# Performance work log

Measured on AMD Instinct MI355X. Metric: run time of the kernel, lower is better.

## Reference

```python
import jax, jax.numpy as jnp
import numpy as np

N_QUBITS = 8
N_LAYERS = 2


def _apply_1q(state, U, wire, n):
    # state: (bs, 2**n); U: (2,2) fixed or (bs,2,2) batched; wire 0 = most significant
    bs = state.shape[0]
    left = 2 ** wire
    right = 2 ** (n - wire - 1)
    s = state.reshape(bs, left, 2, right)
    if U.ndim == 2:
        s = jnp.einsum('ij,bljr->blir', U, s)
    else:
        s = jnp.einsum('bij,bljr->blir', U, s)
    return s.reshape(bs, -1)


def _apply_ctrl(state, U, control, target, n):
    # apply 2x2 U on `target` where `control` qubit is |1>
    bs = state.shape[0]
    left = 2 ** control
    right = 2 ** (n - control - 1)
    s = state.reshape(bs, left, 2, right)
    s0 = s[:, :, 0, :].reshape(bs, -1)
    s1 = s[:, :, 1, :].reshape(bs, -1)
    t = target if target < control else target - 1  # target index among remaining n-1 wires
    s1 = _apply_1q(s1, U, t, n - 1)
    s = jnp.stack([s0.reshape(bs, left, right), s1.reshape(bs, left, right)], axis=2)
    return s.reshape(bs, -1)


def _rz_batched(theta):
    h = 0.5 * theta
    c, s = jnp.cos(h), jnp.sin(h)
    z = jnp.zeros_like(c)
    row0 = jnp.stack([c - 1j * s, z + 0j], axis=-1)
    row1 = jnp.stack([z + 0j, c + 1j * s], axis=-1)
    return jnp.stack([row0, row1], axis=-2).astype(jnp.complex64)  # (bs,2,2)


def _ry_batched(theta):
    h = 0.5 * theta
    c, s = jnp.cos(h), jnp.sin(h)
    row0 = jnp.stack([c, -s], axis=-1)
    row1 = jnp.stack([s, c], axis=-1)
    return jnp.stack([row0, row1], axis=-2).astype(jnp.complex64)


def _rx_fixed(theta):
    h = 0.5 * theta
    c, s = jnp.cos(h), jnp.sin(h)
    return jnp.stack([jnp.stack([c + 0j, -1j * s]), jnp.stack([-1j * s, c + 0j])]).astype(jnp.complex64)


def _ry_fixed(theta):
    h = 0.5 * theta
    c, s = jnp.cos(h), jnp.sin(h)
    return jnp.stack([jnp.stack([c + 0j, -s + 0j]), jnp.stack([s + 0j, c + 0j])]).astype(jnp.complex64)


def _circuit(X, weights):
    bs, L = X.shape
    n = N_QUBITS
    vpq = L // n + 1  # var_per_qubit
    state = jnp.zeros((bs, 2 ** n), jnp.complex64).at[:, 0].set(1.0)
    H = jnp.asarray(np.array([[1, 1], [1, -1]], np.complex64) / np.sqrt(2))
    # encoding: Hadamard then alternating RZ/RY per qubit
    for q in range(n):
        state = _apply_1q(state, H, q, n)
        for i in range(vpq):
            idx = q * vpq + i
            if idx >= L:
                break
            th = X[:, idx]
            U = _rz_batched(th) if i % 2 == 0 else _ry_batched(th)
            state = _apply_1q(state, U, q, n)
    # entangling ring: layer 0 -> CRX, layer 1 -> CRY ((l+1)%2==0 -> CRY)
    for l in range(N_LAYERS):
        for i in range(n):
            th = weights[l, i]
            U = _ry_fixed(th) if (l + 1) % 2 == 0 else _rx_fixed(th)
            state = _apply_ctrl(state, U, i, (i + 1) % n, n)
    # PauliZ expectation on each wire
    p = state.real ** 2 + state.imag ** 2  # (bs, 256)
    outs = []
    for q in range(n):
        pq = p.reshape(bs, 2 ** q, 2, -1).sum(axis=(1, 3))  # (bs, 2)
        outs.append(pq[:, 0] - pq[:, 1])
    return jnp.stack(outs, axis=1)  # (bs, 8)


def setup_inputs() -> dict:
    key = jax.random.key(0)
    k1, k2 = jax.random.split(key)
    X = jax.random.normal(k1, (16384, 64), dtype=jnp.float32)
    weights = jax.random.normal(k2, (N_LAYERS, N_LAYERS * N_QUBITS), dtype=jnp.float32)
    return {"X": X, "weights": weights}


def reference(X, weights):
    return _circuit(X, weights)
```

## Files before the change

### kernel.cpp

```cpp
#include <hip/hip_runtime.h>

#define DEV __device__ __forceinline__
typedef float f32x2 __attribute__((ext_vector_type(2)));
typedef float f32x4 __attribute__((ext_vector_type(4)));

DEV float rdlane(float v, int l) {
  return __int_as_float(__builtin_amdgcn_readlane(__float_as_int(v), l));
}
DEV f32x2 pkfma(f32x2 a, f32x2 b, f32x2 c) { return __builtin_elementwise_fma(a, b, c); }
DEV f32x2 splat(float x) { return (f32x2){x, x}; }
DEV f32x2 swap2(f32x2 v) { return __builtin_shufflevector(v, v, 1, 0); }
DEV f32x2 cmul(f32x2 P, f32x2 F) {
  f32x2 t = swap2(P);
  f32x2 m = {-t.x, t.y};
  return pkfma(splat(F.y), m, splat(F.x) * P);
}

template <int CTRL>
DEV float dppmov(float v) {
  return __int_as_float(__builtin_amdgcn_update_dpp(
      0, __float_as_int(v), CTRL, 0xf, 0xf, true));
}
template <int M>
DEV float xorl(float v) {
  if constexpr (M == 1)       return dppmov<0xB1>(v);
  else if constexpr (M == 2)  return dppmov<0x4E>(v);
  else if constexpr (M == 8)  return dppmov<0x128>(v);
  else if constexpr (M == 4)
    return __int_as_float(__builtin_amdgcn_ds_swizzle(__float_as_int(v), 0x101F));
  else
    return __int_as_float(__builtin_amdgcn_ds_swizzle(__float_as_int(v), 0x401F));
}

template <int M, bool CRX, int R0, int RS>
DEV void gate_lane(f32x2 amp[8], int lane, float c1, float s1) {
  const f32x2 C2 = splat(c1);
  if constexpr (CRX) {
    const f32x2 S2 = {s1, -s1};
#pragma unroll
    for (int r = R0; r < 8; r += RS) {
      f32x2 p;
      p.x = xorl<M>(amp[r].y);
      p.y = xorl<M>(amp[r].x);
      amp[r] = pkfma(S2, p, C2 * amp[r]);
    }
  } else {
    const float sp = (lane & M) ? s1 : -s1;
    const f32x2 SP = splat(sp);
#pragma unroll
    for (int r = R0; r < 8; r += RS) {
      f32x2 p;
      p.x = xorl<M>(amp[r].x);
      p.y = xorl<M>(amp[r].y);
      amp[r] = pkfma(SP, p, C2 * amp[r]);
    }
  }
}

template <bool CRX>
DEV void gate_pair(f32x2& aI, f32x2& aJ, float c1, float s1) {
  const f32x2 C2 = splat(c1);
  f32x2 nI, nJ;
  if constexpr (CRX) {
    const f32x2 S2 = {s1, -s1};
    nI = pkfma(S2, swap2(aJ), C2 * aI);
    nJ = pkfma(S2, swap2(aI), C2 * aJ);
  } else {
    nI = pkfma(splat(-s1), aJ, C2 * aI);
    nJ = pkfma(splat(s1), aI, C2 * aJ);
  }
  aI = nI; aJ = nJ;
}

__global__ __launch_bounds__(256, 8) void qsim_kernel(const float* __restrict__ X,
                                                      const float* __restrict__ W,
                                                      float* __restrict__ out, int bs) {
  const int lane = threadIdx.x & 63;
  const int wave = blockIdx.x * (blockDim.x >> 6) + (threadIdx.x >> 6);
  const int b0 = wave * 2;
  if (b0 >= bs) return;

  float w = W[(((lane & 15) >> 3) << 4) + (lane & 7)];
  float sw, cw;
  __sincosf(0.5f * w, &sw, &cw);

  const int ce = (lane >> 3) & 1;
  const int cq = lane & 7;
  int bb = b0 + ce; bb = bb >= bs ? bs - 1 : bb;
  const float* Xrow = X + (size_t)bb * 64;
  float ang[9];
#pragma unroll
  for (int i = 0; i < 9; ++i) {
    int idx = cq * 9 + i;
    idx = idx > 63 ? 63 : idx;
    ang[i] = Xrow[idx];
  }
  const float Hc = 0.70710678118654752440f;
  f32x2 A = {Hc, 0.f}, B = {Hc, 0.f};
#pragma unroll
  for (int i = 0; i < 9; ++i) {
    float s, c;
    __sincosf(0.5f * ang[i], &s, &c);
    if (i > 0) {
      bool dead = (cq == 7);
      c = dead ? 1.f : c;
      s = dead ? 0.f : s;
    }
    if ((i & 1) == 0) {
      f32x2 nA = pkfma((f32x2){s, -s}, swap2(A), splat(c) * A);
      f32x2 nB = pkfma((f32x2){-s, s}, swap2(B), splat(c) * B);
      A = nA; B = nB;
    } else {
      f32x2 nA = pkfma(splat(-s), B, splat(c) * A);
      f32x2 nB = pkfma(splat(c), B, splat(s) * A);
      A = nA; B = nB;
    }
  }

  __shared__ f32x4 ldsAB[4][16];
  const int wvid = (threadIdx.x >> 6) & 3;
  if (lane < 16) ldsAB[wvid][lane] = (f32x4){A.x, A.y, B.x, B.y};
  __builtin_amdgcn_wave_barrier();

  const int half = lane >> 5;
  const int base = half * 8;
  const f32x2* b2 = (const f32x2*)&ldsAB[wvid][0];
  f32x2 P = b2[(base + 0) * 2 + ((lane >> 4) & 1)];
#pragma unroll
  for (int q = 1; q <= 4; ++q)
    P = cmul(P, b2[(base + q) * 2 + ((lane >> (4 - q)) & 1)]);
  f32x4 F5 = ldsAB[wvid][base + 5];
  f32x4 F6 = ldsAB[wvid][base + 6];
  f32x4 F7 = ldsAB[wvid][base + 7];
  f32x2 A5 = {F5.x, F5.y}, B5 = {F5.z, F5.w};
  f32x2 A6 = {F6.x, F6.y}, B6 = {F6.z, F6.w};
  f32x2 A7 = {F7.x, F7.y}, B7 = {F7.z, F7.w};
  f32x2 amp[8];
  {
    f32x2 t0 = cmul(P, A5), t1 = cmul(P, B5);
    f32x2 u00 = cmul(t0, A6), u01 = cmul(t0, B6);
    f32x2 u10 = cmul(t1, A6), u11 = cmul(t1, B6);
    amp[0] = cmul(u00, A7); amp[1] = cmul(u00, B7);
    amp[2] = cmul(u01, A7); amp[3] = cmul(u01, B7);
    amp[4] = cmul(u10, A7); amp[5] = cmul(u10, B7);
    amp[6] = cmul(u11, A7); amp[7] = cmul(u11, B7);
  }

#pragma unroll
  for (int l = 0; l < 2; ++l) {
    const bool isCRX = (l == 0);
#define CS(G, CBIT) \
    const float cg = rdlane(cw, G), sg = rdlane(sw, G); \
    const bool act = (lane >> (CBIT)) & 1; \
    const float c1 = act ? cg : 1.f, s1 = act ? sg : 0.f;
    { CS(l * 8 + 0, 4)
      if (isCRX) gate_lane<8, true, 0, 1>(amp, lane, c1, s1);
      else       gate_lane<8, false, 0, 1>(amp, lane, c1, s1); }
    { CS(l * 8 + 1, 3)
      if (isCRX) gate_lane<4, true, 0, 1>(amp, lane, c1, s1);
      else       gate_lane<4, false, 0, 1>(amp, lane, c1, s1); }
    { CS(l * 8 + 2, 2)
      if (isCRX) gate_lane<2, true, 0, 1>(amp, lane, c1, s1);
      else       gate_lane<2, false, 0, 1>(amp, lane, c1, s1); }
    { CS(l * 8 + 3, 1)
      if (isCRX) gate_lane<1, true, 0, 1>(amp, lane, c1, s1);
      else       gate_lane<1, false, 0, 1>(amp, lane, c1, s1); }
    { CS(l * 8 + 4, 0)
#pragma unroll
      for (int r = 0; r < 4; ++r) {
        if (isCRX) gate_pair<true>(amp[r], amp[r + 4], c1, s1);
        else       gate_pair<false>(amp[r], amp[r + 4], c1, s1);
      } }
    {
      const float cg = rdlane(cw, l * 8 + 5), sg = rdlane(sw, l * 8 + 5);
      if (isCRX) { gate_pair<true>(amp[4], amp[6], cg, sg);
                   gate_pair<true>(amp[5], amp[7], cg, sg); }
      else       { gate_pair<false>(amp[4], amp[6], cg, sg);
                   gate_pair<false>(amp[5], amp[7], cg, sg); }
    }
    {
      const float cg = rdlane(cw, l * 8 + 6), sg = rdlane(sw, l * 8 + 6);
      if (isCRX) { gate_pair<true>(amp[2], amp[3], cg, sg);
                   gate_pair<true>(amp[6], amp[7], cg, sg); }
      else       { gate_pair<false>(amp[2], amp[3], cg, sg);
                   gate_pair<false>(amp[6], amp[7], cg, sg); }
    }
    {
      const float cg = rdlane(cw, l * 8 + 7), sg = rdlane(sw, l * 8 + 7);
      if (isCRX) gate_lane<16, true, 1, 2>(amp, lane, cg, sg);
      else       gate_lane<16, false, 1, 2>(amp, lane, cg, sg);
    }
#undef CS
  }

  float p[8];
#pragma unroll
  for (int r = 0; r < 8; ++r) p[r] = fmaf(amp[r].x, amp[r].x, amp[r].y * amp[r].y);
  float s01 = p[0] + p[1], s23 = p[2] + p[3], s45 = p[4] + p[5], s67 = p[6] + p[7];
  float sL = s01 + s23, sH = s45 + s67;
  float wv = sL + sH;
  f32x2 D = {sL - sH,
             (s01 + s45) - (s23 + s67)};
  float d7 = (p[0] - p[1]) + (p[2] - p[3]) + (p[4] - p[5]) + (p[6] - p[7]);

#define STAGE(K, M)                                   \
  {                                                   \
    float pp = xorl<M>(wv);                           \
    wv = pp + (((lane >> K) & 1) ? -wv : wv);         \
    f32x2 pd;                                         \
    pd.x = xorl<M>(D.x);                              \
    pd.y = xorl<M>(D.y);                              \
    D = D + pd;                                       \
    d7 += xorl<M>(d7);                                \
  }
  STAGE(0, 1) STAGE(1, 2) STAGE(2, 4) STAGE(3, 8) STAGE(4, 16)
#undef STAGE

  const int lpos = lane & 31;
  const int srcl = (lane & 32) + (16 >> lpos);
  float g = __shfl(wv, srcl, 64);
  float val = (lpos == 5) ? D.x : (lpos == 6) ? D.y : (lpos == 7) ? d7 : g;
  const int brow = b0 + half;
  if (lpos < 8 && brow < bs) out[(size_t)brow * 8 + lpos] = val;
}

extern "C" void kernel_launch(void* const* d_in, const int* in_sizes, int n_in,
                              void* d_out, int out_size, void* d_ws, size_t ws_size,
                              hipStream_t stream) {
  const float* X = (const float*)d_in[0];
  const float* W = (const float*)d_in[1];
  float* out = (float*)d_out;
  int bs = in_sizes[0] / 64;
  int waves = (bs + 1) / 2;
  const int waves_per_block = 4;
  const int threads = waves_per_block * 64;
  int blocks = (waves + waves_per_block - 1) / waves_per_block;
  hipLaunchKernelGGL(qsim_kernel, dim3(blocks), dim3(threads), 0, stream, X, W, out, bs);
}
```

Measured before the change: 64.87 us.

## Replace packed f32x2 math with scalar complex ops and hardware sin/cos intrinsics

Rewrites the complex arithmetic from packed two-float vectors into separate real/imag scalar fmaf chains. It also swaps __sincosf for the raw hardware sin/cos instructions taking revolutions, and hoists all 16 gate cos/sin readlanes into arrays up front. The aim is to drop the shuffle/negate overhead that packed FMA needed for complex multiplies and to cut trig cost. In exchange it gives up dual-issue packed FMA throughput and raises register pressure from the 32 hoisted values.

```diff
diff --git a/kernel.cpp b/kernel.cpp
--- a/kernel.cpp
+++ b/kernel.cpp
@@ -1,21 +1,10 @@
 #include <hip/hip_runtime.h>
 
 #define DEV __device__ __forceinline__
-typedef float f32x2 __attribute__((ext_vector_type(2)));
-typedef float f32x4 __attribute__((ext_vector_type(4)));
 
 DEV float rdlane(float v, int l) {
   return __int_as_float(__builtin_amdgcn_readlane(__float_as_int(v), l));
 }
-DEV f32x2 pkfma(f32x2 a, f32x2 b, f32x2 c) { return __builtin_elementwise_fma(a, b, c); }
-DEV f32x2 splat(float x) { return (f32x2){x, x}; }
-DEV f32x2 swap2(f32x2 v) { return __builtin_shufflevector(v, v, 1, 0); }
-DEV f32x2 cmul(f32x2 P, f32x2 F) {
-  f32x2 t = swap2(P);
-  f32x2 m = {-t.x, t.y};
-  return pkfma(splat(F.y), m, splat(F.x) * P);
-}
-
 template <int CTRL>
 DEV float dppmov(float v) {
   return __int_as_float(__builtin_amdgcn_update_dpp(
@@ -31,45 +20,10 @@
   else
     return __int_as_float(__builtin_amdgcn_ds_swizzle(__float_as_int(v), 0x401F));
 }
-
-template <int M, bool CRX, int R0, int RS>
-DEV void gate_lane(f32x2 amp[8], int lane, float c1, float s1) {
-  const f32x2 C2 = splat(c1);
-  if constexpr (CRX) {
-    const f32x2 S2 = {s1, -s1};
-#pragma unroll
-    for (int r = R0; r < 8; r += RS) {
-      f32x2 p;
-      p.x = xorl<M>(amp[r].y);
-      p.y = xorl<M>(amp[r].x);
-      amp[r] = pkfma(S2, p, C2 * amp[r]);
-    }
-  } else {
-    const float sp = (lane & M) ? s1 : -s1;
-    const f32x2 SP = splat(sp);
-#pragma unroll
-    for (int r = R0; r < 8; r += RS) {
-      f32x2 p;
-      p.x = xorl<M>(amp[r].x);
-      p.y = xorl<M>(amp[r].y);
-      amp[r] = pkfma(SP, p, C2 * amp[r]);
-    }
-  }
-}
-
-template <bool CRX>
-DEV void gate_pair(f32x2& aI, f32x2& aJ, float c1, float s1) {
-  const f32x2 C2 = splat(c1);
-  f32x2 nI, nJ;
-  if constexpr (CRX) {
-    const f32x2 S2 = {s1, -s1};
-    nI = pkfma(S2, swap2(aJ), C2 * aI);
-    nJ = pkfma(S2, swap2(aI), C2 * aJ);
-  } else {
-    nI = pkfma(splat(-s1), aJ, C2 * aI);
-    nJ = pkfma(splat(s1), aI, C2 * aJ);
-  }
-  aI = nI; aJ = nJ;
+DEV void sincos_half(float theta, float* s, float* c) {
+  float rev = theta * 0.07957747154594767f;
+  *s = __builtin_amdgcn_sinf(rev);
+  *c = __builtin_amdgcn_cosf(rev);
 }
 
 __global__ __launch_bounds__(256, 8) void qsim_kernel(const float* __restrict__ X,
@@ -81,8 +35,14 @@
   if (b0 >= bs) return;
 
   float w = W[(((lane & 15) >> 3) << 4) + (lane & 7)];
-  float sw, cw;
-  __sincosf(0.5f * w, &sw, &cw);
+  float sw_, cw_;
+  sincos_half(w, &sw_, &cw_);
+  float CG[16], SG[16];
+#pragma unroll
+  for (int g = 0; g < 16; ++g) { CG[g] = rdlane(cw_, g); SG[g] = rdlane(sw_, g); }
+
+  const bool a4 = (lane >> 4) & 1, a3 = (lane >> 3) & 1, a2 = (lane >> 2) & 1,
+             a1 = (lane >> 1) & 1, a0 = lane & 1;
 
   const int ce = (lane >> 3) & 1;
   const int cq = lane & 7;
@@ -96,121 +56,165 @@
     ang[i] = Xrow[idx];
   }
   const float Hc = 0.70710678118654752440f;
-  f32x2 A = {Hc, 0.f}, B = {Hc, 0.f};
+  float ar = Hc, ai = 0.f, br = Hc, bi = 0.f;
 #pragma unroll
   for (int i = 0; i < 9; ++i) {
     float s, c;
-    __sincosf(0.5f * ang[i], &s, &c);
+    sincos_half(ang[i], &s, &c);
     if (i > 0) {
       bool dead = (cq == 7);
       c = dead ? 1.f : c;
       s = dead ? 0.f : s;
     }
+    float nar, nai, nbr, nbi;
     if ((i & 1) == 0) {
-      f32x2 nA = pkfma((f32x2){s, -s}, swap2(A), splat(c) * A);
-      f32x2 nB = pkfma((f32x2){-s, s}, swap2(B), splat(c) * B);
-      A = nA; B = nB;
+      nar = fmaf(ar, c,  ai * s);  nai = fmaf(ai, c, -ar * s);
+      nbr = fmaf(br, c, -bi * s);  nbi = fmaf(bi, c,  br * s);
     } else {
-      f32x2 nA = pkfma(splat(-s), B, splat(c) * A);
-      f32x2 nB = pkfma(splat(c), B, splat(s) * A);
-      A = nA; B = nB;
+      nar = fmaf(c, ar, -s * br);  nai = fmaf(c, ai, -s * bi);
+      nbr = fmaf(s, ar,  c * br);  nbi = fmaf(s, ai,  c * bi);
     }
-  }
-
-  __shared__ f32x4 ldsAB[4][16];
+    ar = nar; ai = nai; br = nbr; bi = nbi;
+  }
+
+  __shared__ float4 ldsAB[4][16];
   const int wvid = (threadIdx.x >> 6) & 3;
-  if (lane < 16) ldsAB[wvid][lane] = (f32x4){A.x, A.y, B.x, B.y};
+  if (lane < 16) ldsAB[wvid][lane] = make_float4(ar, ai, br, bi);
   __builtin_amdgcn_wave_barrier();
 
   const int half = lane >> 5;
   const int base = half * 8;
-  const f32x2* b2 = (const f32x2*)&ldsAB[wvid][0];
-  f32x2 P = b2[(base + 0) * 2 + ((lane >> 4) & 1)];
-#pragma unroll
-  for (int q = 1; q <= 4; ++q)
-    P = cmul(P, b2[(base + q) * 2 + ((lane >> (4 - q)) & 1)]);
-  f32x4 F5 = ldsAB[wvid][base + 5];
-  f32x4 F6 = ldsAB[wvid][base + 6];
-  f32x4 F7 = ldsAB[wvid][base + 7];
-  f32x2 A5 = {F5.x, F5.y}, B5 = {F5.z, F5.w};
-  f32x2 A6 = {F6.x, F6.y}, B6 = {F6.z, F6.w};
-  f32x2 A7 = {F7.x, F7.y}, B7 = {F7.z, F7.w};
-  f32x2 amp[8];
-  {
-    f32x2 t0 = cmul(P, A5), t1 = cmul(P, B5);
-    f32x2 u00 = cmul(t0, A6), u01 = cmul(t0, B6);
-    f32x2 u10 = cmul(t1, A6), u11 = cmul(t1, B6);
-    amp[0] = cmul(u00, A7); amp[1] = cmul(u00, B7);
-    amp[2] = cmul(u01, A7); amp[3] = cmul(u01, B7);
-    amp[4] = cmul(u10, A7); amp[5] = cmul(u10, B7);
-    amp[6] = cmul(u11, A7); amp[7] = cmul(u11, B7);
-  }
-
-#pragma unroll
-  for (int l = 0; l < 2; ++l) {
-    const bool isCRX = (l == 0);
-#define CS(G, CBIT) \
-    const float cg = rdlane(cw, G), sg = rdlane(sw, G); \
-    const bool act = (lane >> (CBIT)) & 1; \
-    const float c1 = act ? cg : 1.f, s1 = act ? sg : 0.f;
-    { CS(l * 8 + 0, 4)
-      if (isCRX) gate_lane<8, true, 0, 1>(amp, lane, c1, s1);
-      else       gate_lane<8, false, 0, 1>(amp, lane, c1, s1); }
-    { CS(l * 8 + 1, 3)
-      if (isCRX) gate_lane<4, true, 0, 1>(amp, lane, c1, s1);
-      else       gate_lane<4, false, 0, 1>(amp, lane, c1, s1); }
-    { CS(l * 8 + 2, 2)
-      if (isCRX) gate_lane<2, true, 0, 1>(amp, lane, c1, s1);
-      else       gate_lane<2, false, 0, 1>(amp, lane, c1, s1); }
-    { CS(l * 8 + 3, 1)
-      if (isCRX) gate_lane<1, true, 0, 1>(amp, lane, c1, s1);
-      else       gate_lane<1, false, 0, 1>(amp, lane, c1, s1); }
-    { CS(l * 8 + 4, 0)
-#pragma unroll
-      for (int r = 0; r < 4; ++r) {
-        if (isCRX) gate_pair<true>(amp[r], amp[r + 4], c1, s1);
-        else       gate_pair<false>(amp[r], amp[r + 4], c1, s1);
-      } }
-    {
-      const float cg = rdlane(cw, l * 8 + 5), sg = rdlane(sw, l * 8 + 5);
-      if (isCRX) { gate_pair<true>(amp[4], amp[6], cg, sg);
-                   gate_pair<true>(amp[5], amp[7], cg, sg); }
-      else       { gate_pair<false>(amp[4], amp[6], cg, sg);
-                   gate_pair<false>(amp[5], amp[7], cg, sg); }
-    }
-    {
-      const float cg = rdlane(cw, l * 8 + 6), sg = rdlane(sw, l * 8 + 6);
-      if (isCRX) { gate_pair<true>(amp[2], amp[3], cg, sg);
-                   gate_pair<true>(amp[6], amp[7], cg, sg); }
-      else       { gate_pair<false>(amp[2], amp[3], cg, sg);
-                   gate_pair<false>(amp[6], amp[7], cg, sg); }
-    }
-    {
-      const float cg = rdlane(cw, l * 8 + 7), sg = rdlane(sw, l * 8 + 7);
-      if (isCRX) gate_lane<16, true, 1, 2>(amp, lane, cg, sg);
-      else       gate_lane<16, false, 1, 2>(amp, lane, cg, sg);
-    }
-#undef CS
-  }
+  float Pr, Pi;
+  {
+    float4 F0 = ldsAB[wvid][base + 0];
+    Pr = a4 ? F0.z : F0.x;  Pi = a4 ? F0.w : F0.y;
+  }
+#pragma unroll
+  for (int q = 1; q <= 4; ++q) {
+    float4 Fq = ldsAB[wvid][base + q];
+    bool bit = (lane >> (4 - q)) & 1;
+    float fr = bit ? Fq.z : Fq.x, fi = bit ? Fq.w : Fq.y;
+    float nr = fmaf(Pr, fr, -Pi * fi);
+    float ni = fmaf(Pr, fi,  Pi * fr);
+    Pr = nr; Pi = ni;
+  }
+  float4 F5 = ldsAB[wvid][base + 5];
+  float4 F6 = ldsAB[wvid][base + 6];
+  float4 F7 = ldsAB[wvid][base + 7];
+  float re[8], im[8];
+  {
+    float t0r = fmaf(Pr, F5.x, -Pi * F5.y), t0i = fmaf(Pr, F5.y, Pi * F5.x);
+    float t1r = fmaf(Pr, F5.z, -Pi * F5.w), t1i = fmaf(Pr, F5.w, Pi * F5.z);
+    float u00r = fmaf(t0r, F6.x, -t0i * F6.y), u00i = fmaf(t0r, F6.y, t0i * F6.x);
+    float u01r = fmaf(t0r, F6.z, -t0i * F6.w), u01i = fmaf(t0r, F6.w, t0i * F6.z);
+    float u10r = fmaf(t1r, F6.x, -t1i * F6.y), u10i = fmaf(t1r, F6.y, t1i * F6.x);
+    float u11r = fmaf(t1r, F6.z, -t1i * F6.w), u11i = fmaf(t1r, F6.w, t1i * F6.z);
+    re[0] = fmaf(u00r, F7.x, -u00i * F7.y); im[0] = fmaf(u00r, F7.y, u00i * F7.x);
+    re[1] = fmaf(u00r, F7.z, -u00i * F7.w); im[1] = fmaf(u00r, F7.w, u00i * F7.z);
+    re[2] = fmaf(u01r, F7.x, -u01i * F7.y); im[2] = fmaf(u01r, F7.y, u01i * F7.x);
+    re[3] = fmaf(u01r, F7.z, -u01i * F7.w); im[3] = fmaf(u01r, F7.w, u01i * F7.z);
+    re[4] = fmaf(u10r, F7.x, -u10i * F7.y); im[4] = fmaf(u10r, F7.y, u10i * F7.x);
+    re[5] = fmaf(u10r, F7.z, -u10i * F7.w); im[5] = fmaf(u10r, F7.w, u10i * F7.z);
+    re[6] = fmaf(u11r, F7.x, -u11i * F7.y); im[6] = fmaf(u11r, F7.y, u11i * F7.x);
+    re[7] = fmaf(u11r, F7.z, -u11i * F7.w); im[7] = fmaf(u11r, F7.w, u11i * F7.z);
+  }
+
+#define CRX_LANE(M, ACT, G) {                                     \
+    float c1 = (ACT) ? CG[G] : 1.f;                               \
+    float s1 = (ACT) ? SG[G] : 0.f;                               \
+    _Pragma("unroll")                                             \
+    for (int r = 0; r < 8; ++r) {                                 \
+      float pre = xorl<M>(re[r]), pim = xorl<M>(im[r]);           \
+      float nr = fmaf(s1, pim, c1 * re[r]);                       \
+      float ni = fmaf(-s1, pre, c1 * im[r]);                      \
+      re[r] = nr; im[r] = ni;                                     \
+    } }
+#define CRY_LANE(M, ACT, G) {                                     \
+    float c1 = (ACT) ? CG[G] : 1.f;                               \
+    float st = (lane & (M)) ? SG[G] : -SG[G];                     \
+    float sp = (ACT) ? st : 0.f;                                  \
+    _Pragma("unroll")                                             \
+    for (int r = 0; r < 8; ++r) {                                 \
+      float pre = xorl<M>(re[r]), pim = xorl<M>(im[r]);           \
+      float nr = fmaf(sp, pre, c1 * re[r]);                       \
+      float ni = fmaf(sp, pim, c1 * im[r]);                       \
+      re[r] = nr; im[r] = ni;                                     \
+    } }
+#define CRX_M16_ODD(G) {                                          \
+    float c1 = CG[G], s1 = SG[G];                                 \
+    _Pragma("unroll")                                             \
+    for (int r = 1; r < 8; r += 2) {                              \
+      float pre = xorl<16>(re[r]), pim = xorl<16>(im[r]);         \
+      float nr = fmaf(s1, pim, c1 * re[r]);                       \
+      float ni = fmaf(-s1, pre, c1 * im[r]);                      \
+      re[r] = nr; im[r] = ni;                                     \
+    } }
+#define CRY_M16_ODD(G) {                                          \
+    float c1 = CG[G];                                             \
+    float sp = (lane & 16) ? SG[G] : -SG[G];                      \
+    _Pragma("unroll")                                             \
+    for (int r = 1; r < 8; r += 2) {                              \
+      float pre = xorl<16>(re[r]), pim = xorl<16>(im[r]);         \
+      float nr = fmaf(sp, pre, c1 * re[r]);                       \
+      float ni = fmaf(sp, pim, c1 * im[r]);                       \
+      re[r] = nr; im[r] = ni;                                     \
+    } }
+#define PAIR_CRX(I, J, C1, S1) {                                  \
+    float nIr = fmaf((S1), im[J], (C1) * re[I]);                  \
+    float nIi = fmaf(-(S1), re[J], (C1) * im[I]);                 \
+    float nJr = fmaf((S1), im[I], (C1) * re[J]);                  \
+    float nJi = fmaf(-(S1), re[I], (C1) * im[J]);                 \
+    re[I] = nIr; im[I] = nIi; re[J] = nJr; im[J] = nJi; }
+#define PAIR_CRY(I, J, C1, S1) {                                  \
+    float nIr = fmaf(-(S1), re[J], (C1) * re[I]);                 \
+    float nIi = fmaf(-(S1), im[J], (C1) * im[I]);                 \
+    float nJr = fmaf((S1), re[I], (C1) * re[J]);                  \
+    float nJi = fmaf((S1), im[I], (C1) * im[J]);                  \
+    re[I] = nIr; im[I] = nIi; re[J] = nJr; im[J] = nJi; }
+
+  CRX_LANE(8,  a4, 0)
+  CRX_LANE(4,  a3, 1)
+  CRX_LANE(2,  a2, 2)
+  CRX_LANE(1,  a1, 3)
+  {
+    float c1 = a0 ? CG[4] : 1.f;
+    float s1 = a0 ? SG[4] : 0.f;
+    PAIR_CRX(0, 4, c1, s1) PAIR_CRX(1, 5, c1, s1)
+    PAIR_CRX(2, 6, c1, s1) PAIR_CRX(3, 7, c1, s1)
+  }
+  PAIR_CRX(4, 6, CG[5], SG[5]) PAIR_CRX(5, 7, CG[5], SG[5])
+  PAIR_CRX(2, 3, CG[6], SG[6]) PAIR_CRX(6, 7, CG[6], SG[6])
+  CRX_M16_ODD(7)
+
+  CRY_LANE(8,  a4, 8)
+  CRY_LANE(4,  a3, 9)
+  CRY_LANE(2,  a2, 10)
+  CRY_LANE(1,  a1, 11)
+  {
+    float c1 = a0 ? CG[12] : 1.f;
+    float s1 = a0 ? SG[12] : 0.f;
+    PAIR_CRY(0, 4, c1, s1) PAIR_CRY(1, 5, c1, s1)
+    PAIR_CRY(2, 6, c1, s1) PAIR_CRY(3, 7, c1, s1)
+  }
+  PAIR_CRY(4, 6, CG[13], SG[13]) PAIR_CRY(5, 7, CG[13], SG[13])
+  PAIR_CRY(2, 3, CG[14], SG[14]) PAIR_CRY(6, 7, CG[14], SG[14])
+  CRY_M16_ODD(15)
 
   float p[8];
 #pragma unroll
-  for (int r = 0; r < 8; ++r) p[r] = fmaf(amp[r].x, amp[r].x, amp[r].y * amp[r].y);
+  for (int r = 0; r < 8; ++r) p[r] = fmaf(re[r], re[r], im[r] * im[r]);
   float s01 = p[0] + p[1], s23 = p[2] + p[3], s45 = p[4] + p[5], s67 = p[6] + p[7];
   float sL = s01 + s23, sH = s45 + s67;
   float wv = sL + sH;
-  f32x2 D = {sL - sH,
-             (s01 + s45) - (s23 + s67)};
+  float d5 = sL - sH;
+  float d6 = (s01 + s45) - (s23 + s67);
   float d7 = (p[0] - p[1]) + (p[2] - p[3]) + (p[4] - p[5]) + (p[6] - p[7]);
 
-#define STAGE(K, M)                                   \
-  {                                                   \
+#define STAGE(K, M) {                                 \
     float pp = xorl<M>(wv);                           \
     wv = pp + (((lane >> K) & 1) ? -wv : wv);         \
-    f32x2 pd;                                         \
-    pd.x = xorl<M>(D.x);                              \
-    pd.y = xorl<M>(D.y);                              \
-    D = D + pd;                                       \
+    d5 += xorl<M>(d5);                                \
+    d6 += xorl<M>(d6);                                \
     d7 += xorl<M>(d7);                                \
   }
   STAGE(0, 1) STAGE(1, 2) STAGE(2, 4) STAGE(3, 8) STAGE(4, 16)
@@ -219,7 +223,7 @@
   const int lpos = lane & 31;
   const int srcl = (lane & 32) + (16 >> lpos);
   float g = __shfl(wv, srcl, 64);
-  float val = (lpos == 5) ? D.x : (lpos == 6) ? D.y : (lpos == 7) ? d7 : g;
+  float val = (lpos == 5) ? d5 : (lpos == 6) ? d6 : (lpos == 7) ? d7 : g;
   const int brow = b0 + half;
   if (lpos < 8 && brow < bs) out[(size_t)brow * 8 + lpos] = val;
 }
```

Measured after the change: 67.55 us. +4.1%, slower.
